# Optimization experiments

Hardware: AMD Instinct MI355X
Metric: run time of the kernel (lower is better)

The kernel has to match this reference:

```python
import jax, jax.numpy as jnp
import numpy as np

B, K, D, H, ZDIM = 65536, 16, 64, 128, 16

def setup_inputs() -> dict:
    key = jax.random.key(0)
    ks = jax.random.split(key, 20)
    s = 0.05
    inp = {
        'z': jax.random.normal(ks[0], (B, ZDIM), dtype=jnp.float32),
        'y': jax.random.randint(ks[1], (B,), 0, K),
        # backbone: 4 fc blocks (Linear+ReLU)
        'bw0': jax.random.normal(ks[2], (ZDIM, H), dtype=jnp.float32) * s,
        'bb0': jnp.zeros((H,), dtype=jnp.float32),
        'bw1': jax.random.normal(ks[3], (H, H), dtype=jnp.float32) * s,
        'bb1': jnp.zeros((H,), dtype=jnp.float32),
        'bw2': jax.random.normal(ks[4], (H, H), dtype=jnp.float32) * s,
        'bb2': jnp.zeros((H,), dtype=jnp.float32),
        'bw3': jax.random.normal(ks[5], (H, H), dtype=jnp.float32) * s,
        'bb3': jnp.zeros((H,), dtype=jnp.float32),
        # K heads, weights stacked on leading expert axis; layers 0-2 have ReLU, layer 3 does not
        'hw0': jax.random.normal(ks[6], (K, H, H), dtype=jnp.float32) * s,
        'hb0': jnp.zeros((K, H), dtype=jnp.float32),
        'hw1': jax.random.normal(ks[7], (K, H, H), dtype=jnp.float32) * s,
        'hb1': jnp.zeros((K, H), dtype=jnp.float32),
        'hw2': jax.random.normal(ks[8], (K, H, H), dtype=jnp.float32) * s,
        'hb2': jnp.zeros((K, H), dtype=jnp.float32),
        'hw3': jax.random.normal(ks[9], (K, H, D), dtype=jnp.float32) * s,
        'hb3': jnp.zeros((K, D), dtype=jnp.float32),
    }
    return inp

def reference(z, y, bw0, bb0, bw1, bb1, bw2, bb2, bw3, bb3,
              hw0, hb0, hw1, hb1, hw2, hb2, hw3, hb3):
    h = jax.nn.relu(z @ bw0 + bb0)
    h = jax.nn.relu(h @ bw1 + bb1)
    h = jax.nn.relu(h @ bw2 + bb2)
    h = jax.nn.relu(h @ bw3 + bb3)          # [B, H]
    # all K expert heads (faithful to original: compute all, then gather)
    a = jax.nn.relu(jnp.einsum('bi,kij->bkj', h, hw0) + hb0)  # [B, K, H]
    a = jax.nn.relu(jnp.einsum('bki,kij->bkj', a, hw1) + hb1)
    a = jax.nn.relu(jnp.einsum('bki,kij->bkj', a, hw2) + hb2)
    a = jnp.einsum('bki,kij->bkj', a, hw3) + hb3              # [B, K, D], no ReLU
    # select the y-th head per sample
    out = jnp.take_along_axis(a, y[:, None, None], axis=1)[:, 0, :]  # [B, D]
    return out
```

## Files before the change

### kernel.cpp

```cpp
#include <hip/hip_runtime.h>
#include <hip/hip_bf16.h>
#include <stdint.h>


typedef _Float16 f16;
typedef __attribute__((ext_vector_type(2)))  _Float16 f16x2;
typedef __attribute__((ext_vector_type(4)))  _Float16 f16x4;
typedef __attribute__((ext_vector_type(8)))  _Float16 f16x8;
typedef __attribute__((ext_vector_type(16))) float    f32x16;
typedef uint32_t u32;
typedef __attribute__((ext_vector_type(4))) u32 u32x4;

#define MFMA(a, b, c) __builtin_amdgcn_mfma_f32_32x32x16_f16((a), (b), (c), 0, 0, 0)

constexpr int Bc = 65536;
constexpr int Kc = 16;
constexpr int Hc = 128;
constexpr int Dc = 64;

constexpr int CAP  = 4608;
constexpr int SPB  = 128;
constexpr int BPE  = CAP / SPB;
constexpr int NBLK = Kc * BPE;
constexpr int NXCD = 8;
constexpr int CHUNK = NBLK / NXCD;

constexpr float INV_LOSCALE = 1.0f / 1024.0f;

constexpr int BBW_F16 = 2048 + 3 * 16384;
constexpr int HWE_F16 = 3 * 16384 + 8192;

constexpr int PREP_BLKS = 52 + Kc * 56;

struct Act { f16x8 w[8]; };

__device__ __forceinline__ f32x16 zero16() {
    f32x16 z;
#pragma unroll
    for (int i = 0; i < 16; ++i) z[i] = 0.0f;
    return z;
}

__device__ __forceinline__ void gload16(const f16* g, f16* l) {
    __builtin_amdgcn_global_load_lds(
        (const __attribute__((address_space(1))) void*)g,
        (__attribute__((address_space(3))) void*)l, 16, 0, 0);
}

__device__ __forceinline__ void stage_q(f16* dst, const f16* gHi, const f16* gLo,
                                        int wid, int lane) {
#pragma unroll
    for (int i = 0; i < 2; ++i) {
        const int seg = wid * 2 + i;
        gload16(gHi + seg * 512 + lane * 8, dst + seg * 512);
        gload16(gLo + seg * 512 + lane * 8, dst + 4096 + seg * 512);
    }
}

template<bool RELU>
__device__ __forceinline__ void build_windows(
    const f32x16& c0, const f32x16& c1, const float4* bq, int bh,
    f16x8& w0, f16x8& w1)
{
    u32 P[8];
#pragma unroll
    for (int g = 0; g < 4; ++g) {
        const float bb[4] = {bq[g].x, bq[g].y, bq[g].z, bq[g].w};
        f16 h[4];
#pragma unroll
        for (int j = 0; j < 4; ++j) {
            float v = fmaf(c0[4 * g + j] + c1[4 * g + j], INV_LOSCALE, bb[j]);
            if (RELU) v = fmaxf(v, 0.0f);
            h[j] = (f16)v;
        }
        f16x2 p0; p0[0] = h[0]; p0[1] = h[1];
        f16x2 p1; p1[0] = h[2]; p1[1] = h[3];
        P[2 * g]     = __builtin_bit_cast(u32, p0);
        P[2 * g + 1] = __builtin_bit_cast(u32, p1);
    }
    const u32 s0 = (u32)__shfl_xor((int)P[0], 32, 64);
    const u32 s1 = (u32)__shfl_xor((int)P[1], 32, 64);
    const u32 s2 = (u32)__shfl_xor((int)P[2], 32, 64);
    const u32 s3 = (u32)__shfl_xor((int)P[3], 32, 64);
    const u32 s4 = (u32)__shfl_xor((int)P[4], 32, 64);
    const u32 s5 = (u32)__shfl_xor((int)P[5], 32, 64);
    const u32 s6 = (u32)__shfl_xor((int)P[6], 32, 64);
    const u32 s7 = (u32)__shfl_xor((int)P[7], 32, 64);
    const bool hi = (bh != 0);
    u32x4 W0 = { hi ? s2 : P[0], hi ? s3 : P[1], hi ? P[2] : s0, hi ? P[3] : s1 };
    u32x4 W1 = { hi ? s6 : P[4], hi ? s7 : P[5], hi ? P[6] : s4, hi ? P[7] : s5 };
    w0 = __builtin_bit_cast(f16x8, W0);
    w1 = __builtin_bit_cast(f16x8, W1);
}

template<int NQ, bool STAGE_NEXT>
__device__ __forceinline__ void layer_lds(
    f16* lds, int& par, const Act& src, Act& dst,
    const f16* gHi, const f16* gLo, const f16* gHiN, const f16* gLoN,
    const float* __restrict__ biasG, int wid, int lane, int bh)
{
#pragma unroll
    for (int q = 0; q < NQ; ++q) {
        if (q < NQ - 1)
            stage_q(lds + (par ^ 1) * 8192, gHi + (q + 1) * 4096,
                    gLo + (q + 1) * 4096, wid, lane);
        else if (STAGE_NEXT)
            stage_q(lds + (par ^ 1) * 8192, gHiN, gLoN, wid, lane);

        float4 bq[4];
#pragma unroll
        for (int g = 0; g < 4; ++g)
            bq[g] = *(const float4*)(biasG + 32 * q + 8 * g + 4 * bh);

        const f16* pw = lds + par * 8192 + lane * 8;
        f32x16 c0 = zero16(), c1 = zero16();
#pragma unroll
        for (int ks = 0; ks < 8; ++ks) {
            const f16x8 wh = *(const f16x8*)(pw + ks * 512);
            const f16x8 wl = *(const f16x8*)(pw + 4096 + ks * 512);
            c0 = MFMA(wh, src.w[ks], c0);
            c1 = MFMA(wl, src.w[ks], c1);
        }
        build_windows<true>(c0, c1, bq, bh, dst.w[2 * q], dst.w[2 * q + 1]);
        __syncthreads();
        par ^= 1;
    }
}

__device__ __forceinline__ void layer_final(
    f16* lds, int& par, const Act& src,
    const f16* gHi, const f16* gLo, const float* __restrict__ biasG,
    float* __restrict__ out, int bidx, int wid, int lane, int bh)
{
#pragma unroll
    for (int q = 0; q < 2; ++q) {
        if (q == 0)
            stage_q(lds + (par ^ 1) * 8192, gHi + 4096, gLo + 4096, wid, lane);

        float4 bq[4];
#pragma unroll
        for (int g = 0; g < 4; ++g)
            bq[g] = *(const float4*)(biasG + 32 * q + 8 * g + 4 * bh);

        const f16* pw = lds + par * 8192 + lane * 8;
        f32x16 c0 = zero16(), c1 = zero16();
#pragma unroll
        for (int ks = 0; ks < 8; ++ks) {
            const f16x8 wh = *(const f16x8*)(pw + ks * 512);
            const f16x8 wl = *(const f16x8*)(pw + 4096 + ks * 512);
            c0 = MFMA(wh, src.w[ks], c0);
            c1 = MFMA(wl, src.w[ks], c1);
        }
        if (bidx >= 0) {
#pragma unroll
            for (int g = 0; g < 4; ++g) {
                float4 v;
                v.x = fmaf(c0[4 * g + 0] + c1[4 * g + 0], INV_LOSCALE, bq[g].x);
                v.y = fmaf(c0[4 * g + 1] + c1[4 * g + 1], INV_LOSCALE, bq[g].y);
                v.z = fmaf(c0[4 * g + 2] + c1[4 * g + 2], INV_LOSCALE, bq[g].z);
                v.w = fmaf(c0[4 * g + 3] + c1[4 * g + 3], INV_LOSCALE, bq[g].w);
                *(float4*)(out + (size_t)bidx * Dc + 32 * q + 8 * g + 4 * bh) = v;
            }
        }
        if (q == 0) __syncthreads();
        par ^= 1;
    }
}

__global__ __launch_bounds__(256, 3) void fused_mlp(
    const float* __restrict__ z,
    const int* __restrict__ idxb, const int* __restrict__ cursor,
    const f16* __restrict__ bbH, const f16* __restrict__ bbL,
    const float* __restrict__ bb0, const float* __restrict__ bb1,
    const float* __restrict__ bb2, const float* __restrict__ bb3,
    const f16* __restrict__ hH, const f16* __restrict__ hL,
    const float* __restrict__ hb0, const float* __restrict__ hb1,
    const float* __restrict__ hb2, const float* __restrict__ hb3,
    float* __restrict__ out)
{
    __shared__ __attribute__((aligned(16))) f16 WLDS[2 * 8192];

    const int blk = (blockIdx.x % NXCD) * CHUNK + blockIdx.x / NXCD;
    const int e = blk / BPE;
    const int local0 = (blk % BPE) * SPB;
    const int cnt = min(cursor[e * 16], CAP);
    if (cnt - local0 <= 0) return;

    const int tid = threadIdx.x;
    const int wid = tid >> 6, lane = tid & 63;
    const int l31 = lane & 31, bh = lane >> 5;

    int bidx = -1;
    const int sIdx = local0 + wid * 32 + l31;
    if (sIdx < cnt) bidx = idxb[e * CAP + sIdx];

    f16x8 zw;
    if (bidx >= 0) {
        const float4 u0 = *(const float4*)(z + (size_t)bidx * 16 + bh * 8);
        const float4 u1 = *(const float4*)(z + (size_t)bidx * 16 + bh * 8 + 4);
        zw[0] = (f16)u0.x; zw[1] = (f16)u0.y; zw[2] = (f16)u0.z; zw[3] = (f16)u0.w;
        zw[4] = (f16)u1.x; zw[5] = (f16)u1.y; zw[6] = (f16)u1.z; zw[7] = (f16)u1.w;
    } else {
#pragma unroll
        for (int j = 0; j < 8; ++j) zw[j] = (f16)0.0f;
    }

    stage_q(WLDS, bbH + 2048, bbL + 2048, wid, lane);

    Act aA, aB;
#pragma unroll
    for (int q = 0; q < 4; ++q) {
        float4 bq[4];
#pragma unroll
        for (int g = 0; g < 4; ++g)
            bq[g] = *(const float4*)(bb0 + 32 * q + 8 * g + 4 * bh);
        const f16x8 wh = *(const f16x8*)(bbH + q * 512 + lane * 8);
        const f16x8 wl = *(const f16x8*)(bbL + q * 512 + lane * 8);
        f32x16 c0 = zero16(), c1 = zero16();
        c0 = MFMA(wh, zw, c0);
        c1 = MFMA(wl, zw, c1);
        build_windows<true>(c0, c1, bq, bh, aA.w[2 * q], aA.w[2 * q + 1]);
    }
    __syncthreads();
    int par = 0;

    layer_lds<4, true>(WLDS, par, aA, aB, bbH + 2048,  bbL + 2048,
                       bbH + 18432, bbL + 18432, bb1, wid, lane, bh);
    layer_lds<4, true>(WLDS, par, aB, aA, bbH + 18432, bbL + 18432,
                       bbH + 34816, bbL + 34816, bb2, wid, lane, bh);
    const size_t we = (size_t)e * HWE_F16;
    layer_lds<4, true>(WLDS, par, aA, aB, bbH + 34816, bbL + 34816,
                       hH + we, hL + we, bb3, wid, lane, bh);
    layer_lds<4, true>(WLDS, par, aB, aA, hH + we,         hL + we,
                       hH + we + 16384, hL + we + 16384, hb0 + e * Hc, wid, lane, bh);
    layer_lds<4, true>(WLDS, par, aA, aB, hH + we + 16384, hL + we + 16384,
                       hH + we + 32768, hL + we + 32768, hb1 + e * Hc, wid, lane, bh);
    layer_lds<4, true>(WLDS, par, aB, aA, hH + we + 32768, hL + we + 32768,
                       hH + we + 49152, hL + we + 49152, hb2 + e * Hc, wid, lane, bh);
    layer_final(WLDS, par, aA, hH + we + 49152, hL + we + 49152,
                hb3 + e * Dc, out, bidx, wid, lane, bh);
}

__global__ void prep_scatter(
    const float* __restrict__ bw0, const float* __restrict__ bw1,
    const float* __restrict__ bw2, const float* __restrict__ bw3,
    const float* __restrict__ hw0, const float* __restrict__ hw1,
    const float* __restrict__ hw2, const float* __restrict__ hw3,
    f16* __restrict__ bbH, f16* __restrict__ bbL,
    f16* __restrict__ hH,  f16* __restrict__ hL,
    const int* __restrict__ y, int* __restrict__ idxb, int* __restrict__ cursor)
{
    __shared__ float T[32][33];
    __shared__ int lc[Kc];
    __shared__ int lbase[Kc];
    const int id = blockIdx.x;
    const int tx = threadIdx.x;

    if (id >= PREP_BLKS) {
        if (tx < Kc) lc[tx] = 0;
        __syncthreads();
        const int b = (id - PREP_BLKS) * 256 + tx;
        const int e = y[b];
        const int r = atomicAdd(&lc[e], 1);
        __syncthreads();
        if (tx < Kc) lbase[tx] = atomicAdd(&cursor[tx * 16], lc[tx]);
        __syncthreads();
        const int slot = lbase[e] + r;
        if (slot < CAP) idxb[e * CAP + slot] = b;
        return;
    }

    const float* src; f16 *dh, *dl;
    int K, N, k0, n0;
    bool big;

    if (id < 52) {
        if (id < 4) {
            src = bw0; dh = bbH; dl = bbL;
            K = 16; N = 128; k0 = 0; n0 = id * 32; big = false;
        } else {
            const int t = id - 4;
            const int l = t / 16, tile = t % 16;
            const float* bws[3] = {bw1, bw2, bw3};
            src = bws[l];
            dh = bbH + 2048 + l * 16384;
            dl = bbL + 2048 + l * 16384;
            K = 128; N = 128; big = true;
            k0 = (tile >> 2) * 32; n0 = (tile & 3) * 32;
        }
    } else {
        const int t = id - 52;
        const int e = t / 56, r = t % 56;
        if (r < 48) {
            const int l = r / 16, tile = r % 16;
            const float* hws[3] = {hw0, hw1, hw2};
            src = hws[l] + (size_t)e * 16384;
            dh = hH + (size_t)e * HWE_F16 + l * 16384;
            dl = hL + (size_t)e * HWE_F16 + l * 16384;
            K = 128; N = 128; big = true;
            k0 = (tile >> 2) * 32; n0 = (tile & 3) * 32;
        } else {
            const int r2 = r - 48;
            src = hw3 + (size_t)e * 8192;
            dh = hH + (size_t)e * HWE_F16 + 49152;
            dl = hL + (size_t)e * HWE_F16 + 49152;
            K = 128; N = 64; big = true;
            k0 = (r2 >> 1) * 32; n0 = (r2 & 1) * 32;
        }
    }

    const int c = tx & 31, g = tx >> 5;
#pragma unroll
    for (int i = 0; i < 4; ++i) {
        const int row = g * 4 + i;
        if (k0 + row < K)
            T[c][row] = src[(size_t)(k0 + row) * N + n0 + c];
    }
    __syncthreads();
#pragma unroll
    for (int i = 0; i < 4; ++i) {
        const int n = n0 + g * 4 + i;
        const int k = k0 + c;
        if (k < K) {
            const float v = T[g * 4 + i][c];
            const float hif = (float)(f16)v;
            const f16 hi = (f16)(hif * 1024.0f);
            const f16 lo = (f16)((v - hif) * 1024.0f);
            size_t didx;
            if (big)
                didx = (size_t)(n >> 5) * 4096 + (size_t)(k >> 4) * 512
                     + ((k >> 3) & 1) * 256 + (n & 31) * 8 + (k & 7);
            else
                didx = (size_t)(n >> 5) * 512 + (size_t)(k >> 3) * 256
                     + (n & 31) * 8 + (k & 7);
            dh[didx] = hi;
            dl[didx] = lo;
        }
    }
}

extern "C" void kernel_launch(void* const* d_in, const int* in_sizes, int n_in,
                              void* d_out, int out_size, void* d_ws, size_t ws_size,
                              hipStream_t stream)
{
    const float* z   = (const float*)d_in[0];
    const int*   y   = (const int*)d_in[1];
    const float* bw0 = (const float*)d_in[2];
    const float* bb0 = (const float*)d_in[3];
    const float* bw1 = (const float*)d_in[4];
    const float* bb1 = (const float*)d_in[5];
    const float* bw2 = (const float*)d_in[6];
    const float* bb2 = (const float*)d_in[7];
    const float* bw3 = (const float*)d_in[8];
    const float* bb3 = (const float*)d_in[9];
    const float* hw0 = (const float*)d_in[10];
    const float* hb0 = (const float*)d_in[11];
    const float* hw1 = (const float*)d_in[12];
    const float* hb1 = (const float*)d_in[13];
    const float* hw2 = (const float*)d_in[14];
    const float* hb2 = (const float*)d_in[15];
    const float* hw3 = (const float*)d_in[16];
    const float* hb3 = (const float*)d_in[17];
    float* out = (float*)d_out;

    char* p = (char*)d_ws;
    f16* bbH = (f16*)p;  p += (size_t)BBW_F16 * 2;
    f16* bbL = (f16*)p;  p += (size_t)BBW_F16 * 2;
    f16* hH  = (f16*)p;  p += (size_t)Kc * HWE_F16 * 2;
    f16* hL  = (f16*)p;  p += (size_t)Kc * HWE_F16 * 2;
    int* idxb = (int*)p; p += (size_t)Kc * CAP * 4;
    int* cursor = (int*)p;

    hipMemsetAsync(cursor, 0, 256 * sizeof(int), stream);

    prep_scatter<<<PREP_BLKS + Bc / 256, 256, 0, stream>>>(
        bw0, bw1, bw2, bw3, hw0, hw1, hw2, hw3,
        bbH, bbL, hH, hL, y, idxb, cursor);

    fused_mlp<<<NBLK, 256, 0, stream>>>(
        z, idxb, cursor, bbH, bbL, bb0, bb1, bb2, bb3,
        hH, hL, hb0, hb1, hb2, hb3, out);
}
```

Baseline: 144.0 us.

## Process two sample tiles per wave to reuse staged weight fragments

```diff
diff --git a/kernel.cpp b/kernel.cpp
--- a/kernel.cpp
+++ b/kernel.cpp
@@ -50,8 +50,8 @@
 __device__ __forceinline__ void stage_q(f16* dst, const f16* gHi, const f16* gLo,
                                         int wid, int lane) {
 #pragma unroll
-    for (int i = 0; i < 2; ++i) {
-        const int seg = wid * 2 + i;
+    for (int i = 0; i < 4; ++i) {
+        const int seg = wid * 4 + i;
         gload16(gHi + seg * 512 + lane * 8, dst + seg * 512);
         gload16(gLo + seg * 512 + lane * 8, dst + 4096 + seg * 512);
     }
@@ -59,8 +59,7 @@
 
 template<bool RELU>
 __device__ __forceinline__ void build_windows(
-    const f32x16& c0, const f32x16& c1, const float4* bq, int bh,
-    f16x8& w0, f16x8& w1)
+    const f32x16& c, const float4* bq, int bh, f16x8& w0, f16x8& w1)
 {
     u32 P[8];
 #pragma unroll
@@ -69,7 +68,7 @@
         f16 h[4];
 #pragma unroll
         for (int j = 0; j < 4; ++j) {
-            float v = fmaf(c0[4 * g + j] + c1[4 * g + j], INV_LOSCALE, bb[j]);
+            float v = fmaf(c[4 * g + j], INV_LOSCALE, bb[j]);
             if (RELU) v = fmaxf(v, 0.0f);
             h[j] = (f16)v;
         }
@@ -93,73 +92,80 @@
     w1 = __builtin_bit_cast(f16x8, W1);
 }
 
-template<int NQ, bool STAGE_NEXT>
+template<bool STAGE_NEXT>
 __device__ __forceinline__ void layer_lds(
-    f16* lds, int& par, const Act& src, Act& dst,
+    f16* lds, int& par, const Act& s0, const Act& s1, Act& d0, Act& d1,
     const f16* gHi, const f16* gLo, const f16* gHiN, const f16* gLoN,
     const float* __restrict__ biasG, int wid, int lane, int bh)
 {
 #pragma unroll
-    for (int q = 0; q < NQ; ++q) {
-        if (q < NQ - 1)
+    for (int q = 0; q < 4; ++q) {
+        if (q < 3)
             stage_q(lds + (par ^ 1) * 8192, gHi + (q + 1) * 4096,
                     gLo + (q + 1) * 4096, wid, lane);
         else if (STAGE_NEXT)
             stage_q(lds + (par ^ 1) * 8192, gHiN, gLoN, wid, lane);
 
-        float4 bq[4];
-#pragma unroll
-        for (int g = 0; g < 4; ++g)
-            bq[g] = *(const float4*)(biasG + 32 * q + 8 * g + 4 * bh);
-
         const f16* pw = lds + par * 8192 + lane * 8;
         f32x16 c0 = zero16(), c1 = zero16();
 #pragma unroll
         for (int ks = 0; ks < 8; ++ks) {
             const f16x8 wh = *(const f16x8*)(pw + ks * 512);
             const f16x8 wl = *(const f16x8*)(pw + 4096 + ks * 512);
-            c0 = MFMA(wh, src.w[ks], c0);
-            c1 = MFMA(wl, src.w[ks], c1);
-        }
-        build_windows<true>(c0, c1, bq, bh, dst.w[2 * q], dst.w[2 * q + 1]);
+            c0 = MFMA(wh, s0.w[ks], c0);
+            c1 = MFMA(wh, s1.w[ks], c1);
+            c0 = MFMA(wl, s0.w[ks], c0);
+            c1 = MFMA(wl, s1.w[ks], c1);
+        }
+        float4 bq[4];
+#pragma unroll
+        for (int g = 0; g < 4; ++g)
+            bq[g] = *(const float4*)(biasG + 32 * q + 8 * g + 4 * bh);
+        build_windows<true>(c0, bq, bh, d0.w[2 * q], d0.w[2 * q + 1]);
+        build_windows<true>(c1, bq, bh, d1.w[2 * q], d1.w[2 * q + 1]);
         __syncthreads();
         par ^= 1;
     }
 }
 
 __device__ __forceinline__ void layer_final(
-    f16* lds, int& par, const Act& src,
+    f16* lds, int& par, const Act& s0, const Act& s1,
     const f16* gHi, const f16* gLo, const float* __restrict__ biasG,
-    float* __restrict__ out, int bidx, int wid, int lane, int bh)
+    float* __restrict__ out, int bidx0, int bidx1, int wid, int lane, int bh)
 {
 #pragma unroll
     for (int q = 0; q < 2; ++q) {
         if (q == 0)
             stage_q(lds + (par ^ 1) * 8192, gHi + 4096, gLo + 4096, wid, lane);
 
-        float4 bq[4];
-#pragma unroll
-        for (int g = 0; g < 4; ++g)
-            bq[g] = *(const float4*)(biasG + 32 * q + 8 * g + 4 * bh);
-
         const f16* pw = lds + par * 8192 + lane * 8;
         f32x16 c0 = zero16(), c1 = zero16();
 #pragma unroll
         for (int ks = 0; ks < 8; ++ks) {
             const f16x8 wh = *(const f16x8*)(pw + ks * 512);
             const f16x8 wl = *(const f16x8*)(pw + 4096 + ks * 512);
-            c0 = MFMA(wh, src.w[ks], c0);
-            c1 = MFMA(wl, src.w[ks], c1);
-        }
-        if (bidx >= 0) {
+            c0 = MFMA(wh, s0.w[ks], c0);
+            c1 = MFMA(wh, s1.w[ks], c1);
+            c0 = MFMA(wl, s0.w[ks], c0);
+            c1 = MFMA(wl, s1.w[ks], c1);
+        }
+        float4 bq[4];
+#pragma unroll
+        for (int g = 0; g < 4; ++g)
+            bq[g] = *(const float4*)(biasG + 32 * q + 8 * g + 4 * bh);
+#pragma unroll
+        for (int mt = 0; mt < 2; ++mt) {
+            const int b = mt ? bidx1 : bidx0;
+            if (b < 0) continue;
+            const f32x16& ac = mt ? c1 : c0;
 #pragma unroll
             for (int g = 0; g < 4; ++g) {
                 float4 v;
-                v.x = fmaf(c0[4 * g + 0] + c1[4 * g + 0], INV_LOSCALE, bq[g].x);
-                v.y = fmaf(c0[4 * g + 1] + c1[4 * g + 1], INV_LOSCALE, bq[g].y);
-                v.z = fmaf(c0[4 * g + 2] + c1[4 * g + 2], INV_LOSCALE, bq[g].z);
-                v.w = fmaf(c0[4 * g + 3] + c1[4 * g + 3], INV_LOSCALE, bq[g].w);
-                *(float4*)(out + (size_t)bidx * Dc + 32 * q + 8 * g + 4 * bh) = v;
+                v.x = fmaf(ac[4 * g + 0], INV_LOSCALE, bq[g].x);
+                v.y = fmaf(ac[4 * g + 1], INV_LOSCALE, bq[g].y);
+                v.z = fmaf(ac[4 * g + 2], INV_LOSCALE, bq[g].z);
+                v.w = fmaf(ac[4 * g + 3], INV_LOSCALE, bq[g].w);
+                *(float4*)(out + (size_t)b * Dc + 32 * q + 8 * g + 4 * bh) = v;
             }
         }
         if (q == 0) __syncthreads();
@@ -167,7 +173,7 @@
     }
 }
 
-__global__ __launch_bounds__(256, 3) void fused_mlp(
+__global__ __launch_bounds__(128, 2) void fused_mlp(
     const float* __restrict__ z,
     const int* __restrict__ idxb, const int* __restrict__ cursor,
     const f16* __restrict__ bbH, const f16* __restrict__ bbL,
@@ -190,55 +196,64 @@
     const int wid = tid >> 6, lane = tid & 63;
     const int l31 = lane & 31, bh = lane >> 5;
 
-    int bidx = -1;
-    const int sIdx = local0 + wid * 32 + l31;
-    if (sIdx < cnt) bidx = idxb[e * CAP + sIdx];
-
-    f16x8 zw;
-    if (bidx >= 0) {
-        const float4 u0 = *(const float4*)(z + (size_t)bidx * 16 + bh * 8);
-        const float4 u1 = *(const float4*)(z + (size_t)bidx * 16 + bh * 8 + 4);
-        zw[0] = (f16)u0.x; zw[1] = (f16)u0.y; zw[2] = (f16)u0.z; zw[3] = (f16)u0.w;
-        zw[4] = (f16)u1.x; zw[5] = (f16)u1.y; zw[6] = (f16)u1.z; zw[7] = (f16)u1.w;
-    } else {
-#pragma unroll
-        for (int j = 0; j < 8; ++j) zw[j] = (f16)0.0f;
+    const int sBase = local0 + wid * 64;
+    int bidx0 = -1, bidx1 = -1;
+    if (sBase + l31 < cnt)      bidx0 = idxb[e * CAP + sBase + l31];
+    if (sBase + 32 + l31 < cnt) bidx1 = idxb[e * CAP + sBase + 32 + l31];
+
+    f16x8 zw0, zw1;
+#pragma unroll
+    for (int j = 0; j < 8; ++j) { zw0[j] = (f16)0.0f; zw1[j] = (f16)0.0f; }
+    if (bidx0 >= 0) {
+        const float4 u0 = *(const float4*)(z + (size_t)bidx0 * 16 + bh * 8);
+        const float4 u1 = *(const float4*)(z + (size_t)bidx0 * 16 + bh * 8 + 4);
+        zw0[0] = (f16)u0.x; zw0[1] = (f16)u0.y; zw0[2] = (f16)u0.z; zw0[3] = (f16)u0.w;
+        zw0[4] = (f16)u1.x; zw0[5] = (f16)u1.y; zw0[6] = (f16)u1.z; zw0[7] = (f16)u1.w;
+    }
+    if (bidx1 >= 0) {
+        const float4 u0 = *(const float4*)(z + (size_t)bidx1 * 16 + bh * 8);
+        const float4 u1 = *(const float4*)(z + (size_t)bidx1 * 16 + bh * 8 + 4);
+        zw1[0] = (f16)u0.x; zw1[1] = (f16)u0.y; zw1[2] = (f16)u0.z; zw1[3] = (f16)u0.w;
+        zw1[4] = (f16)u1.x; zw1[5] = (f16)u1.y; zw1[6] = (f16)u1.z; zw1[7] = (f16)u1.w;
     }
 
     stage_q(WLDS, bbH + 2048, bbL + 2048, wid, lane);
 
-    Act aA, aB;
+    Act aA0, aA1, aB0, aB1;
 #pragma unroll
     for (int q = 0; q < 4; ++q) {
-        float4 bq[4];
-#pragma unroll
-        for (int g = 0; g < 4; ++g)
-            bq[g] = *(const float4*)(bb0 + 32 * q + 8 * g + 4 * bh);
         const f16x8 wh = *(const f16x8*)(bbH + q * 512 + lane * 8);
         const f16x8 wl = *(const f16x8*)(bbL + q * 512 + lane * 8);
         f32x16 c0 = zero16(), c1 = zero16();
-        c0 = MFMA(wh, zw, c0);
-        c1 = MFMA(wl, zw, c1);
-        build_windows<true>(c0, c1, bq, bh, aA.w[2 * q], aA.w[2 * q + 1]);
+        c0 = MFMA(wh, zw0, c0);
+        c1 = MFMA(wh, zw1, c1);
+        c0 = MFMA(wl, zw0, c0);
+        c1 = MFMA(wl, zw1, c1);
+        float4 bq[4];
+#pragma unroll
+        for (int g = 0; g < 4; ++g)
+            bq[g] = *(const float4*)(bb0 + 32 * q + 8 * g + 4 * bh);
+        build_windows<true>(c0, bq, bh, aA0.w[2 * q], aA0.w[2 * q + 1]);
+        build_windows<true>(c1, bq, bh, aA1.w[2 * q], aA1.w[2 * q + 1]);
     }
     __syncthreads();
     int par = 0;
 
-    layer_lds<4, true>(WLDS, par, aA, aB, bbH + 2048,  bbL + 2048,
-                       bbH + 18432, bbL + 18432, bb1, wid, lane, bh);
-    layer_lds<4, true>(WLDS, par, aB, aA, bbH + 18432, bbL + 18432,
-                       bbH + 34816, bbL + 34816, bb2, wid, lane, bh);
+    layer_lds<true>(WLDS, par, aA0, aA1, aB0, aB1, bbH + 2048,  bbL + 2048,
+                    bbH + 18432, bbL + 18432, bb1, wid, lane, bh);
+    layer_lds<true>(WLDS, par, aB0, aB1, aA0, aA1, bbH + 18432, bbL + 18432,
+                    bbH + 34816, bbL + 34816, bb2, wid, lane, bh);
     const size_t we = (size_t)e * HWE_F16;
-    layer_lds<4, true>(WLDS, par, aA, aB, bbH + 34816, bbL + 34816,
-                       hH + we, hL + we, bb3, wid, lane, bh);
-    layer_lds<4, true>(WLDS, par, aB, aA, hH + we,         hL + we,
-                       hH + we + 16384, hL + we + 16384, hb0 + e * Hc, wid, lane, bh);
-    layer_lds<4, true>(WLDS, par, aA, aB, hH + we + 16384, hL + we + 16384,
-                       hH + we + 32768, hL + we + 32768, hb1 + e * Hc, wid, lane, bh);
-    layer_lds<4, true>(WLDS, par, aB, aA, hH + we + 32768, hL + we + 32768,
-                       hH + we + 49152, hL + we + 49152, hb2 + e * Hc, wid, lane, bh);
-    layer_final(WLDS, par, aA, hH + we + 49152, hL + we + 49152,
-                hb3 + e * Dc, out, bidx, wid, lane, bh);
+    layer_lds<true>(WLDS, par, aA0, aA1, aB0, aB1, bbH + 34816, bbL + 34816,
+                    hH + we, hL + we, bb3, wid, lane, bh);
+    layer_lds<true>(WLDS, par, aB0, aB1, aA0, aA1, hH + we,         hL + we,
+                    hH + we + 16384, hL + we + 16384, hb0 + e * Hc, wid, lane, bh);
+    layer_lds<true>(WLDS, par, aA0, aA1, aB0, aB1, hH + we + 16384, hL + we + 16384,
+                    hH + we + 32768, hL + we + 32768, hb1 + e * Hc, wid, lane, bh);
+    layer_lds<true>(WLDS, par, aB0, aB1, aA0, aA1, hH + we + 32768, hL + we + 32768,
+                    hH + we + 49152, hL + we + 49152, hb2 + e * Hc, wid, lane, bh);
+    layer_final(WLDS, par, aA0, aA1, hH + we + 49152, hL + we + 49152,
+                hb3 + e * Dc, out, bidx0, bidx1, wid, lane, bh);
 }
 
 __global__ void prep_scatter(
@@ -377,7 +392,7 @@
         bw0, bw1, bw2, bw3, hw0, hw1, hw2, hw3,
         bbH, bbL, hH, hL, y, idxb, cursor);
 
-    fused_mlp<<<NBLK, 256, 0, stream>>>(
+    fused_mlp<<<NBLK, 128, 0, stream>>>(
         z, idxb, cursor, bbH, bbL, bb0, bb1, bb2, bb3,
         hH, hL, hb0, hb1, hb2, hb3, out);
 }
```

After: 147.8 us. 1.03x slower.
